# Performance work log

Hardware: AMD Instinct MI355X
Metric: run time of the kernel (lower is better)

Reference implementation:

```python
import jax, jax.numpy as jnp
import numpy as np

K = 3
PAD = K // 2


def conv3x3(x, w, b):
    # x: [B,C,H,W], w: [O,C,3,3], b: [O]
    y = jax.lax.conv_general_dilated(
        x, w, window_strides=(1, 1), padding=[(1, 1), (1, 1)],
        dimension_numbers=("NCHW", "OIHW", "NCHW"))
    return y + b[None, :, None, None]


def bilinear_gather(x, py, px):
    # x: [B,C,H,W]; py, px: [B,KK,H,W] float sample coords -> [B,C,KK,H,W]
    B, C, H, W = x.shape
    y0f = jnp.floor(py)
    x0f = jnp.floor(px)
    ly = (py - y0f)[:, None]  # [B,1,KK,H,W]
    lx = (px - x0f)[:, None]
    y0 = y0f.astype(jnp.int32)
    x0 = x0f.astype(jnp.int32)

    def gather(yi, xi):
        valid = ((yi >= 0) & (yi < H) & (xi >= 0) & (xi < W))
        yc = jnp.clip(yi, 0, H - 1)
        xc = jnp.clip(xi, 0, W - 1)
        # per-batch fancy gather: [C,H,W][: , idx, idx] -> [C,KK,H,W]
        g = jax.vmap(lambda xb, yb, xb2: xb[:, yb, xb2])(x, yc, xc)
        return g * valid[:, None].astype(x.dtype)

    v00 = gather(y0, x0)
    v01 = gather(y0, x0 + 1)
    v10 = gather(y0 + 1, x0)
    v11 = gather(y0 + 1, x0 + 1)
    return (v00 * (1 - ly) * (1 - lx) + v01 * (1 - ly) * lx
            + v10 * ly * (1 - lx) + v11 * ly * lx)


def setup_inputs() -> dict:
    key = jax.random.key(0)
    ks = jax.random.split(key, 7)
    B, C, H, W = 8, 128, 64, 64
    KK = K * K
    s_in = 1.0 / np.sqrt(C * KK)
    s3 = 1.0 / np.sqrt(C * 9)
    return {
        "x": jax.random.normal(ks[0], (B, C, H, W), jnp.float32),
        "offset_w": jax.random.normal(ks[1], (2 * KK, C, 3, 3), jnp.float32) * s3,
        "offset_b": jax.random.normal(ks[2], (2 * KK,), jnp.float32) * 0.01,
        "mask_w": jax.random.normal(ks[3], (KK, C, 3, 3), jnp.float32) * s3,
        "mask_b": jax.random.normal(ks[4], (KK,), jnp.float32) * 0.01,
        "weight": jax.random.normal(ks[5], (C, C, K, K), jnp.float32) * s_in,
        "bias": jax.random.normal(ks[6], (C,), jnp.float32) * 0.01,
    }


def reference(x, offset_w, offset_b, mask_w, mask_b, weight, bias):
    B, C, H, W = x.shape
    KK = K * K
    offset = conv3x3(x, offset_w, offset_b)            # [B,2*KK,H,W]
    mask = jax.nn.sigmoid(conv3x3(x, mask_w, mask_b))  # [B,KK,H,W]
    off = offset.reshape(B, KK, 2, H, W)
    dy, dx = off[:, :, 0], off[:, :, 1]                # torchvision: (dy, dx) per tap

    ky = (jnp.arange(KK, dtype=jnp.float32) // K) - PAD  # [KK] kernel row offsets
    kx = (jnp.arange(KK, dtype=jnp.float32) % K) - PAD
    py = jnp.arange(H, dtype=jnp.float32)[None, None, :, None] + ky[None, :, None, None] + dy
    px = jnp.arange(W, dtype=jnp.float32)[None, None, None, :] + kx[None, :, None, None] + dx

    sampled = bilinear_gather(x, py, px)               # [B,C,KK,H,W]
    sampled = sampled * mask[:, None]
    y = jnp.einsum("bckhw,ock->bohw", sampled, weight.reshape(C, C, KK))
    return y + bias[None, :, None, None]
```

## Files before the change

kernel.cpp:

```cpp
#include <hip/hip_runtime.h>
#include <math.h>

#define BATCH 8
#define CH    128
#define HH    64
#define WW    64
#define HWSZ  (HH*WW)
#define KK    9
#define OC27  27
#define KDIM  1152

typedef unsigned short ushort_t;
typedef unsigned int   uint_t;
typedef __attribute__((ext_vector_type(8))) short  short8v;
typedef __attribute__((ext_vector_type(4))) float  float4v;

__device__ __forceinline__ float bf2f(uint_t u16) {
    return __uint_as_float(u16 << 16);
}
__device__ __forceinline__ float bf2f_hi(uint_t u) {
    return __uint_as_float(u & 0xffff0000u);
}
__device__ __forceinline__ ushort_t f2bf(float f) {
    uint_t u = __float_as_uint(f);
    return (ushort_t)((u + 0x7fffu + ((u >> 16) & 1u)) >> 16);
}

__global__ void k_prep_x(const float* __restrict__ in, ushort_t* __restrict__ out) {
    __shared__ float tile[32][33];
    int b  = blockIdx.z;
    int c0 = blockIdx.y * 32;
    int s0 = blockIdx.x * 32;
    int tx = threadIdx.x, ty = threadIdx.y;
    const float* inb = in  + (size_t)b * CH * HWSZ;
    ushort_t*   outb = out + (size_t)b * HWSZ * CH;
#pragma unroll
    for (int i = 0; i < 32; i += 8)
        tile[ty + i][tx] = inb[(size_t)(c0 + ty + i) * HWSZ + s0 + tx];
    __syncthreads();
#pragma unroll
    for (int i = 0; i < 32; i += 8)
        outb[(size_t)(s0 + ty + i) * CH + c0 + tx] = f2bf(tile[tx][ty + i]);
}

__global__ __launch_bounds__(256) void k_prep_w(const float* __restrict__ weight,
                                                ushort_t* __restrict__ w2) {
    int e = blockIdx.x * 256 + threadIdx.x;
    if (e >= CH * KDIM) return;
    int oc  = e / KDIM;
    int rem = e - oc * KDIM;
    int c   = rem / KK;
    int t   = rem - c * KK;
    int k_lin = (c >> 5) * 288 + t * 32 + (c & 31);
    w2[(size_t)(k_lin >> 3) * (CH * 8) + oc * 8 + (k_lin & 7)] = f2bf(weight[e]);
}

__global__ __launch_bounds__(256) void k_prep_w_om(const float* __restrict__ offset_w,
                                                   const float* __restrict__ mask_w,
                                                   ushort_t* __restrict__ w2om) {
    int e = blockIdx.x * 256 + threadIdx.x;
    if (e >= 32 * KDIM) return;
    int oc  = e / KDIM;
    int rem = e - oc * KDIM;
    int c   = rem / KK;
    int t   = rem - c * KK;
    float v = 0.f;
    if (oc < 18)      v = offset_w[(size_t)oc * KDIM + rem];
    else if (oc < 27) v = mask_w[(size_t)(oc - 18) * KDIM + rem];
    int k_lin = (c >> 5) * 288 + t * 32 + (c & 31);
    w2om[(size_t)(k_lin >> 3) * (32 * 8) + oc * 8 + (k_lin & 7)] = f2bf(v);
}

#define DP   64
#define RSE  320

__device__ __forceinline__ int swz(int row, int off) { return off ^ ((row & 7) << 3); }

__global__ __launch_bounds__(256) void k_fused(
        const ushort_t* __restrict__ x_bf,
        const ushort_t* __restrict__ w2,
        const ushort_t* __restrict__ w2om,
        const float* __restrict__ offset_b, const float* __restrict__ mask_b,
        const float* __restrict__ bias,
        float* __restrict__ out) {
    __shared__ ushort_t s[DP * RSE];
    __shared__ float    psf[2880];

    int tid = threadIdx.x;
    int p0  = blockIdx.x * DP;
    int b   = p0 >> 12;
    int h   = (p0 >> 6) & 63;
    int wid = tid >> 6, lane = tid & 63;
    int lh  = lane >> 4, ll = lane & 15;

    const ushort_t* xb_img = x_bf + ((size_t)b * HWSZ * CH);

    float4v acc1[2];
    acc1[0] = (float4v){0.f, 0.f, 0.f, 0.f};
    acc1[1] = (float4v){0.f, 0.f, 0.f, 0.f};

    for (int chunk = 0; chunk < 4; ++chunk) {
        int c0 = chunk * 32;
#pragma unroll
        for (int i = 0; i < 9; ++i) {
            int v   = tid + i * 256;
            int t   = v >> 8;
            int r   = v & 255;
            int pix = r >> 2, cg = r & 3;
            int y   = h + t / 3 - 1;
            int x   = pix + t % 3 - 1;
            uint4 u = make_uint4(0u, 0u, 0u, 0u);
            if (y >= 0 && y < HH && x >= 0 && x < WW)
                u = *(const uint4*)(xb_img + (size_t)(y * WW + x) * CH + c0 + cg * 8);
            *(uint4*)(&s[pix * RSE + swz(pix, t * 32 + cg * 8)]) = u;
        }
        __syncthreads();

        const ushort_t* wb = w2om + (size_t)chunk * 36 * 256;
#pragma unroll 3
        for (int ks = 0; ks < 9; ++ks) {
            int row = wid * 16 + ll;
            short8v a = *(const short8v*)(&s[row * RSE + swz(row, ks * 32 + lh * 8)]);
            const ushort_t* wp = wb + (ks * 4 + lh) * 256 + ll * 8;
            short8v b0 = *(const short8v*)(wp);
            short8v b1 = *(const short8v*)(wp + 128);
            acc1[0] = __builtin_amdgcn_mfma_f32_16x16x32_bf16(a, b0, acc1[0], 0, 0, 0);
            acc1[1] = __builtin_amdgcn_mfma_f32_16x16x32_bf16(a, b1, acc1[1], 0, 0, 0);
        }
        __syncthreads();
    }

#pragma unroll
    for (int j = 0; j < 2; ++j) {
        int oc = j * 16 + ll;
        if (oc < OC27) {
            float bv = (oc < 18) ? offset_b[oc] : mask_b[oc - 18];
#pragma unroll
            for (int r = 0; r < 4; ++r) {
                int pix = wid * 16 + lh * 4 + r;
                float vv = acc1[j][r] + bv;
                if (oc >= 18) vv = 1.f / (1.f + expf(-vv));
                psf[pix * 27 + oc] = vv;
            }
        }
    }
    __syncthreads();

    float dy0 = 0.f, dx0 = 0.f, m0 = 0.f, dy1 = 0.f, dx1 = 0.f, m1 = 0.f;
    float dy2 = 0.f, dx2 = 0.f, m2 = 0.f;
    {
        int v0 = tid,      pA = v0 / 9, tA = v0 - pA * 9;
        int v1 = tid + 256, pB = v1 / 9, tB = v1 - pB * 9;
        dy0 = psf[pA * 27 + 2 * tA]; dx0 = psf[pA * 27 + 2 * tA + 1]; m0 = psf[pA * 27 + 18 + tA];
        dy1 = psf[pB * 27 + 2 * tB]; dx1 = psf[pB * 27 + 2 * tB + 1]; m1 = psf[pB * 27 + 18 + tB];
        if (tid < 64) {
            int v2 = tid + 512, pC = v2 / 9, tC = v2 - pC * 9;
            dy2 = psf[pC * 27 + 2 * tC]; dx2 = psf[pC * 27 + 2 * tC + 1]; m2 = psf[pC * 27 + 18 + tC];
        }
    }
    __syncthreads();

    uint_t* enc = (uint_t*)(psf + 2304);
#define PARAM_STORE(v, dy, dx, m) {                                             \
        int pix = (v) / 9, t = (v) - pix * 9;                                   \
        float py = (float)(h + t / 3 - 1) + (dy);                               \
        float px = (float)(pix + t % 3 - 1) + (dx);                             \
        float y0f = floorf(py), x0f = floorf(px);                               \
        float ly = py - y0f, lx = px - x0f;                                     \
        int y0 = (int)y0f, x0 = (int)x0f;                                       \
        int y1 = y0 + 1,   x1 = x0 + 1;                                         \
        bool vy0 = (y0 >= 0) & (y0 < HH), vy1 = (y1 >= 0) & (y1 < HH);          \
        bool vx0 = (x0 >= 0) & (x0 < WW), vx1 = (x1 >= 0) & (x1 < WW);          \
        int yc0 = min(max(y0, 0), HH - 1), yc1 = min(max(y1, 0), HH - 1);       \
        int xc0 = min(max(x0, 0), WW - 1), xc1 = min(max(x1, 0), WW - 1);       \
        int idx00 = (yc0 * WW + xc0) * CH;                                      \
        enc[v] = (uint_t)idx00 | ((uint_t)(xc1 - xc0) << 30)                    \
                               | ((uint_t)(yc1 - yc0) << 31);                   \
        float4 wq;                                                              \
        wq.x = (1.f - ly) * (1.f - lx) * (m) * ((vy0 && vx0) ? 1.f : 0.f);      \
        wq.y = (1.f - ly) * lx         * (m) * ((vy0 && vx1) ? 1.f : 0.f);      \
        wq.z = ly         * (1.f - lx) * (m) * ((vy1 && vx0) ? 1.f : 0.f);      \
        wq.w = ly         * lx         * (m) * ((vy1 && vx1) ? 1.f : 0.f);      \
        *(float4*)(&psf[(v) * 4]) = wq;                                         \
    }
    PARAM_STORE(tid,       dy0, dx0, m0);
    PARAM_STORE(tid + 256, dy1, dx1, m1);
    if (tid < 64) PARAM_STORE(tid + 512, dy2, dx2, m2);
#undef PARAM_STORE
    __syncthreads();

    int wr = wid & 1;
    int wc = wid >> 1;
    float4v acc[2][4];
#pragma unroll
    for (int i = 0; i < 2; i++)
#pragma unroll
        for (int j = 0; j < 4; j++)
            acc[i][j] = (float4v){0.f, 0.f, 0.f, 0.f};

    for (int chunk = 0; chunk < 4; ++chunk) {
        int c0 = chunk * 32;
#pragma unroll
        for (int i = 0; i < 9; ++i) {
            int v   = tid + i * 256;
            int t   = v >> 8;
            int r   = v & 255;
            int pix = r >> 2, cg = r & 3;
            int pv  = pix * 9 + t;
            uint_t e  = enc[pv];
            float4 wq = *(const float4*)(&psf[pv * 4]);
            int idx00 = (int)(e & 0x3FFFFFFFu);
            int dxo   = (int)((e >> 30) & 1u) << 7;
            int dyo   = (int)(e >> 31) << 13;
            const ushort_t* bp = xb_img + idx00 + c0 + cg * 8;
            uint4 u00 = *(const uint4*)(bp);
            uint4 u01 = *(const uint4*)(bp + dxo);
            uint4 u10 = *(const uint4*)(bp + dyo);
            uint4 u11 = *(const uint4*)(bp + dxo + dyo);
            uint4 res;
#define CMB(fld) {                                                         \
            float lo = wq.x * bf2f(u00.fld & 0xffffu);                     \
            lo = fmaf(wq.y, bf2f(u01.fld & 0xffffu), lo);                  \
            lo = fmaf(wq.z, bf2f(u10.fld & 0xffffu), lo);                  \
            lo = fmaf(wq.w, bf2f(u11.fld & 0xffffu), lo);                  \
            float hi = wq.x * bf2f_hi(u00.fld);                            \
            hi = fmaf(wq.y, bf2f_hi(u01.fld), hi);                        \
            hi = fmaf(wq.z, bf2f_hi(u10.fld), hi);                        \
            hi = fmaf(wq.w, bf2f_hi(u11.fld), hi);                        \
            res.fld = (uint_t)f2bf(lo) | ((uint_t)f2bf(hi) << 16); }
            CMB(x); CMB(y); CMB(z); CMB(w);
#undef CMB
            *(uint4*)(&s[pix * RSE + swz(pix, t * 32 + cg * 8)]) = res;
        }
        __syncthreads();

        const ushort_t* wb = w2 + (size_t)chunk * 36 * 1024;
        __builtin_amdgcn_s_setprio(1);
#pragma unroll 3
        for (int ks = 0; ks < 9; ++ks) {
            int rowA = wr * 32 + ll;
            int off  = swz(rowA, ks * 32 + lh * 8);
            short8v a0 = *(const short8v*)(&s[rowA * RSE + off]);
            short8v a1 = *(const short8v*)(&s[(rowA + 16) * RSE + off]);
            const ushort_t* wp = wb + (ks * 4 + lh) * 1024 + (wc * 64 + ll) * 8;
            short8v b0 = *(const short8v*)(wp);
            short8v b1 = *(const short8v*)(wp + 128);
            short8v b2 = *(const short8v*)(wp + 256);
            short8v b3 = *(const short8v*)(wp + 384);
            acc[0][0] = __builtin_amdgcn_mfma_f32_16x16x32_bf16(a0, b0, acc[0][0], 0, 0, 0);
            acc[0][1] = __builtin_amdgcn_mfma_f32_16x16x32_bf16(a0, b1, acc[0][1], 0, 0, 0);
            acc[0][2] = __builtin_amdgcn_mfma_f32_16x16x32_bf16(a0, b2, acc[0][2], 0, 0, 0);
            acc[0][3] = __builtin_amdgcn_mfma_f32_16x16x32_bf16(a0, b3, acc[0][3], 0, 0, 0);
            acc[1][0] = __builtin_amdgcn_mfma_f32_16x16x32_bf16(a1, b0, acc[1][0], 0, 0, 0);
            acc[1][1] = __builtin_amdgcn_mfma_f32_16x16x32_bf16(a1, b1, acc[1][1], 0, 0, 0);
            acc[1][2] = __builtin_amdgcn_mfma_f32_16x16x32_bf16(a1, b2, acc[1][2], 0, 0, 0);
            acc[1][3] = __builtin_amdgcn_mfma_f32_16x16x32_bf16(a1, b3, acc[1][3], 0, 0, 0);
        }
        __builtin_amdgcn_s_setprio(0);
        __syncthreads();
    }

#pragma unroll
    for (int pi = 0; pi < 2; ++pi) {
#pragma unroll
        for (int oj = 0; oj < 4; ++oj) {
            int oc = wc * 64 + oj * 16 + ll;
            int w  = wr * 32 + pi * 16 + lh * 4;
            float bv = bias[oc];
            float4v a = acc[pi][oj];
            float* op = out + (((size_t)(b * CH + oc)) << 12) + (h << 6) + w;
            *(float4*)op = make_float4(a[0] + bv, a[1] + bv, a[2] + bv, a[3] + bv);
        }
    }
}

extern "C" void kernel_launch(void* const* d_in, const int* in_sizes, int n_in,
                              void* d_out, int out_size, void* d_ws, size_t ws_size,
                              hipStream_t stream) {
    const float* x        = (const float*)d_in[0];
    const float* offset_w = (const float*)d_in[1];
    const float* offset_b = (const float*)d_in[2];
    const float* mask_w   = (const float*)d_in[3];
    const float* mask_b   = (const float*)d_in[4];
    const float* weight   = (const float*)d_in[5];
    const float* bias     = (const float*)d_in[6];
    float* out = (float*)d_out;

    char* ws = (char*)d_ws;
    ushort_t* x_bf = (ushort_t*)ws;
    ushort_t* w2   = (ushort_t*)(ws + 8388608);
    ushort_t* w2om = (ushort_t*)(ws + 8388608 + 294912);

    dim3 tb(32, 8, 1);
    dim3 tg(HWSZ / 32, CH / 32, BATCH);
    k_prep_x<<<tg, tb, 0, stream>>>(x, x_bf);
    k_prep_w<<<(CH * KDIM + 255) / 256, 256, 0, stream>>>(weight, w2);
    k_prep_w_om<<<(32 * KDIM + 255) / 256, 256, 0, stream>>>(offset_w, mask_w, w2om);

    int npix = BATCH * HWSZ;
    k_fused<<<npix / DP, 256, 0, stream>>>(x_bf, w2, w2om, offset_b, mask_b, bias, out);
}
```

Measured before the change: 61.98 us.

## Prefetch next channel chunk into registers during MFMA in both GEMM phases

Both the offset/mask conv phase and the deformable GEMM phase now issue global loads for the next 32-channel chunk into registers before the MFMA loop, then write them to shared memory after the barrier. The goal is to hide gather latency behind matrix compute. The thread-to-pixel mapping is simplified, and launch_bounds now requests 2 blocks per CU. This adds many live registers: 36 uint4 for the bilinear prefetch, which risks spills or lower occupancy.

```diff
diff --git a/kernel.cpp b/kernel.cpp
--- a/kernel.cpp
+++ b/kernel.cpp
@@ -76,7 +76,7 @@
 
 __device__ __forceinline__ int swz(int row, int off) { return off ^ ((row & 7) << 3); }
 
-__global__ __launch_bounds__(256) void k_fused(
+__global__ __launch_bounds__(256, 2) void k_fused(
         const ushort_t* __restrict__ x_bf,
         const ushort_t* __restrict__ w2,
         const ushort_t* __restrict__ w2om,
@@ -95,39 +95,58 @@
 
     const ushort_t* xb_img = x_bf + ((size_t)b * HWSZ * CH);
 
+    int pixS = tid >> 2, cgS = tid & 3;
+
     float4v acc1[2];
     acc1[0] = (float4v){0.f, 0.f, 0.f, 0.f};
     acc1[1] = (float4v){0.f, 0.f, 0.f, 0.f};
 
-    for (int chunk = 0; chunk < 4; ++chunk) {
-        int c0 = chunk * 32;
+    {
+        uint4 pf1[9];
 #pragma unroll
         for (int i = 0; i < 9; ++i) {
-            int v   = tid + i * 256;
-            int t   = v >> 8;
-            int r   = v & 255;
-            int pix = r >> 2, cg = r & 3;
-            int y   = h + t / 3 - 1;
-            int x   = pix + t % 3 - 1;
+            int y = h + i / 3 - 1;
+            int x = pixS + i % 3 - 1;
             uint4 u = make_uint4(0u, 0u, 0u, 0u);
             if (y >= 0 && y < HH && x >= 0 && x < WW)
-                u = *(const uint4*)(xb_img + (size_t)(y * WW + x) * CH + c0 + cg * 8);
-            *(uint4*)(&s[pix * RSE + swz(pix, t * 32 + cg * 8)]) = u;
-        }
-        __syncthreads();
-
-        const ushort_t* wb = w2om + (size_t)chunk * 36 * 256;
+                u = *(const uint4*)(xb_img + (size_t)(y * WW + x) * CH + cgS * 8);
+            *(uint4*)(&s[pixS * RSE + swz(pixS, i * 32 + cgS * 8)]) = u;
+        }
+        for (int chunk = 0; chunk < 4; ++chunk) {
+            __syncthreads();
+            if (chunk < 3) {
+                int c0n = (chunk + 1) * 32;
+#pragma unroll
+                for (int i = 0; i < 9; ++i) {
+                    int y = h + i / 3 - 1;
+                    int x = pixS + i % 3 - 1;
+                    int yc = min(max(y, 0), HH - 1), xc = min(max(x, 0), WW - 1);
+                    pf1[i] = *(const uint4*)(xb_img + (size_t)(yc * WW + xc) * CH + c0n + cgS * 8);
+                }
+            }
+            const ushort_t* wb = w2om + (size_t)chunk * 36 * 256;
 #pragma unroll 3
-        for (int ks = 0; ks < 9; ++ks) {
-            int row = wid * 16 + ll;
-            short8v a = *(const short8v*)(&s[row * RSE + swz(row, ks * 32 + lh * 8)]);
-            const ushort_t* wp = wb + (ks * 4 + lh) * 256 + ll * 8;
-            short8v b0 = *(const short8v*)(wp);
-            short8v b1 = *(const short8v*)(wp + 128);
-            acc1[0] = __builtin_amdgcn_mfma_f32_16x16x32_bf16(a, b0, acc1[0], 0, 0, 0);
-            acc1[1] = __builtin_amdgcn_mfma_f32_16x16x32_bf16(a, b1, acc1[1], 0, 0, 0);
-        }
-        __syncthreads();
+            for (int ks = 0; ks < 9; ++ks) {
+                int row = wid * 16 + ll;
+                short8v a = *(const short8v*)(&s[row * RSE + swz(row, ks * 32 + lh * 8)]);
+                const ushort_t* wp = wb + (ks * 4 + lh) * 256 + ll * 8;
+                short8v b0 = *(const short8v*)(wp);
+                short8v b1 = *(const short8v*)(wp + 128);
+                acc1[0] = __builtin_amdgcn_mfma_f32_16x16x32_bf16(a, b0, acc1[0], 0, 0, 0);
+                acc1[1] = __builtin_amdgcn_mfma_f32_16x16x32_bf16(a, b1, acc1[1], 0, 0, 0);
+            }
+            __syncthreads();
+            if (chunk < 3) {
+#pragma unroll
+                for (int i = 0; i < 9; ++i) {
+                    int y = h + i / 3 - 1;
+                    int x = pixS + i % 3 - 1;
+                    bool valid = (y >= 0) && (y < HH) && (x >= 0) && (x < WW);
+                    uint4 u = valid ? pf1[i] : make_uint4(0u, 0u, 0u, 0u);
+                    *(uint4*)(&s[pixS * RSE + swz(pixS, i * 32 + cgS * 8)]) = u;
+                }
+            }
+        }
     }
 
 #pragma unroll
@@ -198,26 +217,6 @@
         for (int j = 0; j < 4; j++)
             acc[i][j] = (float4v){0.f, 0.f, 0.f, 0.f};
 
-    for (int chunk = 0; chunk < 4; ++chunk) {
-        int c0 = chunk * 32;
-#pragma unroll
-        for (int i = 0; i < 9; ++i) {
-            int v   = tid + i * 256;
-            int t   = v >> 8;
-            int r   = v & 255;
-            int pix = r >> 2, cg = r & 3;
-            int pv  = pix * 9 + t;
-            uint_t e  = enc[pv];
-            float4 wq = *(const float4*)(&psf[pv * 4]);
-            int idx00 = (int)(e & 0x3FFFFFFFu);
-            int dxo   = (int)((e >> 30) & 1u) << 7;
-            int dyo   = (int)(e >> 31) << 13;
-            const ushort_t* bp = xb_img + idx00 + c0 + cg * 8;
-            uint4 u00 = *(const uint4*)(bp);
-            uint4 u01 = *(const uint4*)(bp + dxo);
-            uint4 u10 = *(const uint4*)(bp + dyo);
-            uint4 u11 = *(const uint4*)(bp + dxo + dyo);
-            uint4 res;
 #define CMB(fld) {                                                         \
             float lo = wq.x * bf2f(u00.fld & 0xffffu);                     \
             lo = fmaf(wq.y, bf2f(u01.fld & 0xffffu), lo);                  \
@@ -228,37 +227,84 @@
             hi = fmaf(wq.z, bf2f_hi(u10.fld), hi);                        \
             hi = fmaf(wq.w, bf2f_hi(u11.fld), hi);                        \
             res.fld = (uint_t)f2bf(lo) | ((uint_t)f2bf(hi) << 16); }
+
+    {
+        uint4 pf[9][4];
+#pragma unroll
+        for (int i = 0; i < 9; ++i) {
+            int pv  = pixS * 9 + i;
+            uint_t e  = enc[pv];
+            float4 wq = *(const float4*)(&psf[pv * 4]);
+            int idx00 = (int)(e & 0x3FFFFFFFu);
+            int dxo   = (int)((e >> 30) & 1u) << 7;
+            int dyo   = (int)(e >> 31) << 13;
+            const ushort_t* bp = xb_img + idx00 + cgS * 8;
+            uint4 u00 = *(const uint4*)(bp);
+            uint4 u01 = *(const uint4*)(bp + dxo);
+            uint4 u10 = *(const uint4*)(bp + dyo);
+            uint4 u11 = *(const uint4*)(bp + dxo + dyo);
+            uint4 res;
             CMB(x); CMB(y); CMB(z); CMB(w);
+            *(uint4*)(&s[pixS * RSE + swz(pixS, i * 32 + cgS * 8)]) = res;
+        }
+        for (int chunk = 0; chunk < 4; ++chunk) {
+            __syncthreads();
+            if (chunk < 3) {
+                int c0n = (chunk + 1) * 32;
+#pragma unroll
+                for (int i = 0; i < 9; ++i) {
+                    uint_t e  = enc[pixS * 9 + i];
+                    int idx00 = (int)(e & 0x3FFFFFFFu);
+                    int dxo   = (int)((e >> 30) & 1u) << 7;
+                    int dyo   = (int)(e >> 31) << 13;
+                    const ushort_t* bp = xb_img + idx00 + c0n + cgS * 8;
+                    pf[i][0] = *(const uint4*)(bp);
+                    pf[i][1] = *(const uint4*)(bp + dxo);
+                    pf[i][2] = *(const uint4*)(bp + dyo);
+                    pf[i][3] = *(const uint4*)(bp + dxo + dyo);
+                }
+            }
+            const ushort_t* wb = w2 + (size_t)chunk * 36 * 1024;
+            __builtin_amdgcn_s_setprio(1);
+#pragma unroll 3
+            for (int ks = 0; ks < 9; ++ks) {
+                int rowA = wr * 32 + ll;
+                int off  = swz(rowA, ks * 32 + lh * 8);
+                short8v a0 = *(const short8v*)(&s[rowA * RSE + off]);
+                short8v a1 = *(const short8v*)(&s[(rowA + 16) * RSE + off]);
+                const ushort_t* wp = wb + (ks * 4 + lh) * 1024 + (wc * 64 + ll) * 8;
+                short8v b0 = *(const short8v*)(wp);
+                short8v b1 = *(const short8v*)(wp + 128);
+                short8v b2 = *(const short8v*)(wp + 256);
+                short8v b3 = *(const short8v*)(wp + 384);
+                acc[0][0] = __builtin_amdgcn_mfma_f32_16x16x32_bf16(a0, b0, acc[0][0], 0, 0, 0);
+                acc[0][1] = __builtin_amdgcn_mfma_f32_16x16x32_bf16(a0, b1, acc[0][1], 0, 0, 0);
+                acc[0][2] = __builtin_amdgcn_mfma_f32_16x16x32_bf16(a0, b2, acc[0][2], 0, 0, 0);
+                acc[0][3] = __builtin_amdgcn_mfma_f32_16x16x32_bf16(a0, b3, acc[0][3], 0, 0, 0);
+                acc[1][0] = __builtin_amdgcn_mfma_f32_16x16x32_bf16(a1, b0, acc[1][0], 0, 0, 0);
+                acc[1][1] = __builtin_amdgcn_mfma_f32_16x16x32_bf16(a1, b1, acc[1][1], 0, 0, 0);
+                acc[1][2] = __builtin_amdgcn_mfma_f32_16x16x32_bf16(a1, b2, acc[1][2], 0, 0, 0);
+                acc[1][3] = __builtin_amdgcn_mfma_f32_16x16x32_bf16(a1, b3, acc[1][3], 0, 0, 0);
+            }
+            __builtin_amdgcn_s_setprio(0);
+            __syncthreads();
+            if (chunk < 3) {
+#pragma unroll
+                for (int i = 0; i < 9; ++i) {
+                    int pv = pixS * 9 + i;
+                    float4 wq = *(const float4*)(&psf[pv * 4]);
+                    uint4 u00 = pf[i][0];
+                    uint4 u01 = pf[i][1];
+                    uint4 u10 = pf[i][2];
+                    uint4 u11 = pf[i][3];
+                    uint4 res;
+                    CMB(x); CMB(y); CMB(z); CMB(w);
+                    *(uint4*)(&s[pixS * RSE + swz(pixS, i * 32 + cgS * 8)]) = res;
+                }
+            }
+        }
+    }
 #undef CMB
-            *(uint4*)(&s[pix * RSE + swz(pix, t * 32 + cg * 8)]) = res;
-        }
-        __syncthreads();
-
-        const ushort_t* wb = w2 + (size_t)chunk * 36 * 1024;
-        __builtin_amdgcn_s_setprio(1);
-#pragma unroll 3
-        for (int ks = 0; ks < 9; ++ks) {
-            int rowA = wr * 32 + ll;
-            int off  = swz(rowA, ks * 32 + lh * 8);
-            short8v a0 = *(const short8v*)(&s[rowA * RSE + off]);
-            short8v a1 = *(const short8v*)(&s[(rowA + 16) * RSE + off]);
-            const ushort_t* wp = wb + (ks * 4 + lh) * 1024 + (wc * 64 + ll) * 8;
-            short8v b0 = *(const short8v*)(wp);
-            short8v b1 = *(const short8v*)(wp + 128);
-            short8v b2 = *(const short8v*)(wp + 256);
-            short8v b3 = *(const short8v*)(wp + 384);
-            acc[0][0] = __builtin_amdgcn_mfma_f32_16x16x32_bf16(a0, b0, acc[0][0], 0, 0, 0);
-            acc[0][1] = __builtin_amdgcn_mfma_f32_16x16x32_bf16(a0, b1, acc[0][1], 0, 0, 0);
-            acc[0][2] = __builtin_amdgcn_mfma_f32_16x16x32_bf16(a0, b2, acc[0][2], 0, 0, 0);
-            acc[0][3] = __builtin_amdgcn_mfma_f32_16x16x32_bf16(a0, b3, acc[0][3], 0, 0, 0);
-            acc[1][0] = __builtin_amdgcn_mfma_f32_16x16x32_bf16(a1, b0, acc[1][0], 0, 0, 0);
-            acc[1][1] = __builtin_amdgcn_mfma_f32_16x16x32_bf16(a1, b1, acc[1][1], 0, 0, 0);
-            acc[1][2] = __builtin_amdgcn_mfma_f32_16x16x32_bf16(a1, b2, acc[1][2], 0, 0, 0);
-            acc[1][3] = __builtin_amdgcn_mfma_f32_16x16x32_bf16(a1, b3, acc[1][3], 0, 0, 0);
-        }
-        __builtin_amdgcn_s_setprio(0);
-        __syncthreads();
-    }
 
 #pragma unroll
     for (int pi = 0; pi < 2; ++pi) {
```

After: 61.10 us. Within noise of the previous version (-1.4%).

## Split output channels across two blocks and merge weight prep kernels

Applied to the files above, without the earlier changes.

The fused kernel now launches twice as many blocks, with each block handling half of the output channels (64) for its 64 pixels. Each wave now computes 16 pixels by 64 channels instead of 32 by 64, which halves accumulator registers and should raise occupancy and block-level parallelism. The cost is that each block pair repeats the offset/mask convolution and the bilinear gather, so that work is done twice. The two weight-prep kernels are also merged into one launch to save launch overhead.

```diff
diff --git a/kernel.cpp b/kernel.cpp
--- a/kernel.cpp
+++ b/kernel.cpp
@@ -43,32 +43,31 @@
         outb[(size_t)(s0 + ty + i) * CH + c0 + tx] = f2bf(tile[tx][ty + i]);
 }
 
-__global__ __launch_bounds__(256) void k_prep_w(const float* __restrict__ weight,
-                                                ushort_t* __restrict__ w2) {
+__global__ __launch_bounds__(256) void k_prep_wb(const float* __restrict__ weight,
+                                                 const float* __restrict__ offset_w,
+                                                 const float* __restrict__ mask_w,
+                                                 ushort_t* __restrict__ w2,
+                                                 ushort_t* __restrict__ w2om) {
     int e = blockIdx.x * 256 + threadIdx.x;
-    if (e >= CH * KDIM) return;
-    int oc  = e / KDIM;
-    int rem = e - oc * KDIM;
-    int c   = rem / KK;
-    int t   = rem - c * KK;
-    int k_lin = (c >> 5) * 288 + t * 32 + (c & 31);
-    w2[(size_t)(k_lin >> 3) * (CH * 8) + oc * 8 + (k_lin & 7)] = f2bf(weight[e]);
-}
-
-__global__ __launch_bounds__(256) void k_prep_w_om(const float* __restrict__ offset_w,
-                                                   const float* __restrict__ mask_w,
-                                                   ushort_t* __restrict__ w2om) {
-    int e = blockIdx.x * 256 + threadIdx.x;
-    if (e >= 32 * KDIM) return;
-    int oc  = e / KDIM;
-    int rem = e - oc * KDIM;
-    int c   = rem / KK;
-    int t   = rem - c * KK;
-    float v = 0.f;
-    if (oc < 18)      v = offset_w[(size_t)oc * KDIM + rem];
-    else if (oc < 27) v = mask_w[(size_t)(oc - 18) * KDIM + rem];
-    int k_lin = (c >> 5) * 288 + t * 32 + (c & 31);
-    w2om[(size_t)(k_lin >> 3) * (32 * 8) + oc * 8 + (k_lin & 7)] = f2bf(v);
+    if (e < CH * KDIM) {
+        int oc  = e / KDIM;
+        int rem = e - oc * KDIM;
+        int c   = rem / KK;
+        int t   = rem - c * KK;
+        int k_lin = (c >> 5) * 288 + t * 32 + (c & 31);
+        w2[(size_t)(k_lin >> 3) * (CH * 8) + oc * 8 + (k_lin & 7)] = f2bf(weight[e]);
+    } else if (e < CH * KDIM + 32 * KDIM) {
+        int e2  = e - CH * KDIM;
+        int oc  = e2 / KDIM;
+        int rem = e2 - oc * KDIM;
+        int c   = rem / KK;
+        int t   = rem - c * KK;
+        float v = 0.f;
+        if (oc < 18)      v = offset_w[(size_t)oc * KDIM + rem];
+        else if (oc < 27) v = mask_w[(size_t)(oc - 18) * KDIM + rem];
+        int k_lin = (c >> 5) * 288 + t * 32 + (c & 31);
+        w2om[(size_t)(k_lin >> 3) * (32 * 8) + oc * 8 + (k_lin & 7)] = f2bf(v);
+    }
 }
 
 #define DP   64
@@ -189,14 +188,12 @@
 #undef PARAM_STORE
     __syncthreads();
 
-    int wr = wid & 1;
-    int wc = wid >> 1;
-    float4v acc[2][4];
-#pragma unroll
-    for (int i = 0; i < 2; i++)
-#pragma unroll
-        for (int j = 0; j < 4; j++)
-            acc[i][j] = (float4v){0.f, 0.f, 0.f, 0.f};
+    int wr = wid;
+    int wc = blockIdx.y;
+    float4v acc[4];
+#pragma unroll
+    for (int j = 0; j < 4; j++)
+        acc[j] = (float4v){0.f, 0.f, 0.f, 0.f};
 
     for (int chunk = 0; chunk < 4; ++chunk) {
         int c0 = chunk * 32;
@@ -238,39 +235,30 @@
         __builtin_amdgcn_s_setprio(1);
 #pragma unroll 3
         for (int ks = 0; ks < 9; ++ks) {
-            int rowA = wr * 32 + ll;
-            int off  = swz(rowA, ks * 32 + lh * 8);
-            short8v a0 = *(const short8v*)(&s[rowA * RSE + off]);
-            short8v a1 = *(const short8v*)(&s[(rowA + 16) * RSE + off]);
+            int rowA = wr * 16 + ll;
+            short8v a0 = *(const short8v*)(&s[rowA * RSE + swz(rowA, ks * 32 + lh * 8)]);
             const ushort_t* wp = wb + (ks * 4 + lh) * 1024 + (wc * 64 + ll) * 8;
             short8v b0 = *(const short8v*)(wp);
             short8v b1 = *(const short8v*)(wp + 128);
             short8v b2 = *(const short8v*)(wp + 256);
             short8v b3 = *(const short8v*)(wp + 384);
-            acc[0][0] = __builtin_amdgcn_mfma_f32_16x16x32_bf16(a0, b0, acc[0][0], 0, 0, 0);
-            acc[0][1] = __builtin_amdgcn_mfma_f32_16x16x32_bf16(a0, b1, acc[0][1], 0, 0, 0);
-            acc[0][2] = __builtin_amdgcn_mfma_f32_16x16x32_bf16(a0, b2, acc[0][2], 0, 0, 0);
-            acc[0][3] = __builtin_amdgcn_mfma_f32_16x16x32_bf16(a0, b3, acc[0][3], 0, 0, 0);
-            acc[1][0] = __builtin_amdgcn_mfma_f32_16x16x32_bf16(a1, b0, acc[1][0], 0, 0, 0);
-            acc[1][1] = __builtin_amdgcn_mfma_f32_16x16x32_bf16(a1, b1, acc[1][1], 0, 0, 0);
-            acc[1][2] = __builtin_amdgcn_mfma_f32_16x16x32_bf16(a1, b2, acc[1][2], 0, 0, 0);
-            acc[1][3] = __builtin_amdgcn_mfma_f32_16x16x32_bf16(a1, b3, acc[1][3], 0, 0, 0);
+            acc[0] = __builtin_amdgcn_mfma_f32_16x16x32_bf16(a0, b0, acc[0], 0, 0, 0);
+            acc[1] = __builtin_amdgcn_mfma_f32_16x16x32_bf16(a0, b1, acc[1], 0, 0, 0);
+            acc[2] = __builtin_amdgcn_mfma_f32_16x16x32_bf16(a0, b2, acc[2], 0, 0, 0);
+            acc[3] = __builtin_amdgcn_mfma_f32_16x16x32_bf16(a0, b3, acc[3], 0, 0, 0);
         }
         __builtin_amdgcn_s_setprio(0);
         __syncthreads();
     }
 
 #pragma unroll
-    for (int pi = 0; pi < 2; ++pi) {
-#pragma unroll
-        for (int oj = 0; oj < 4; ++oj) {
-            int oc = wc * 64 + oj * 16 + ll;
-            int w  = wr * 32 + pi * 16 + lh * 4;
-            float bv = bias[oc];
-            float4v a = acc[pi][oj];
-            float* op = out + (((size_t)(b * CH + oc)) << 12) + (h << 6) + w;
-            *(float4*)op = make_float4(a[0] + bv, a[1] + bv, a[2] + bv, a[3] + bv);
-        }
+    for (int oj = 0; oj < 4; ++oj) {
+        int oc = wc * 64 + oj * 16 + ll;
+        int w  = wr * 16 + lh * 4;
+        float bv = bias[oc];
+        float4v a = acc[oj];
+        float* op = out + (((size_t)(b * CH + oc)) << 12) + (h << 6) + w;
+        *(float4*)op = make_float4(a[0] + bv, a[1] + bv, a[2] + bv, a[3] + bv);
     }
 }
 
@@ -294,9 +282,9 @@
     dim3 tb(32, 8, 1);
     dim3 tg(HWSZ / 32, CH / 32, BATCH);
     k_prep_x<<<tg, tb, 0, stream>>>(x, x_bf);
-    k_prep_w<<<(CH * KDIM + 255) / 256, 256, 0, stream>>>(weight, w2);
-    k_prep_w_om<<<(32 * KDIM + 255) / 256, 256, 0, stream>>>(offset_w, mask_w, w2om);
+    k_prep_wb<<<((CH + 32) * KDIM + 255) / 256, 256, 0, stream>>>(weight, offset_w, mask_w, w2, w2om);
 
     int npix = BATCH * HWSZ;
-    k_fused<<<npix / DP, 256, 0, stream>>>(x_bf, w2, w2om, offset_b, mask_b, bias, out);
-}
+    dim3 fg(npix / DP, 2, 1);
+    k_fused<<<fg, 256, 0, stream>>>(x_bf, w2, w2om, offset_b, mask_b, bias, out);
+}
```

After: 99.22 us. +60.1%, slower.

## Merge prep kernels into one launch and stage halo rows for offset conv

Applied to the files above, without the earlier changes.

Combines the three preprocessing kernels (x transpose to bf16, weight reorder, offset/mask weight reorder) into a single launch, removing two kernel launch gaps. In the fused kernel, the offset/mask conv no longer stages a 9x im2col copy of the input. It loads three halo rows of 66 pixels once per channel chunk into a padded shared layout and indexes taps by row and column shift. This cuts global loads and LDS writes per chunk, at the cost of an unswizzled padded-stride layout that may cause LDS bank conflicts.

```diff
diff --git a/kernel.cpp b/kernel.cpp
--- a/kernel.cpp
+++ b/kernel.cpp
@@ -26,53 +26,56 @@
     return (ushort_t)((u + 0x7fffu + ((u >> 16) & 1u)) >> 16);
 }
 
-__global__ void k_prep_x(const float* __restrict__ in, ushort_t* __restrict__ out) {
+__global__ __launch_bounds__(256) void k_prep_all(const float* __restrict__ in,
+                                                  const float* __restrict__ weight,
+                                                  const float* __restrict__ offset_w,
+                                                  const float* __restrict__ mask_w,
+                                                  ushort_t* __restrict__ x_bf,
+                                                  ushort_t* __restrict__ w2,
+                                                  ushort_t* __restrict__ w2om) {
     __shared__ float tile[32][33];
-    int b  = blockIdx.z;
-    int c0 = blockIdx.y * 32;
-    int s0 = blockIdx.x * 32;
-    int tx = threadIdx.x, ty = threadIdx.y;
-    const float* inb = in  + (size_t)b * CH * HWSZ;
-    ushort_t*   outb = out + (size_t)b * HWSZ * CH;
-#pragma unroll
-    for (int i = 0; i < 32; i += 8)
-        tile[ty + i][tx] = inb[(size_t)(c0 + ty + i) * HWSZ + s0 + tx];
-    __syncthreads();
-#pragma unroll
-    for (int i = 0; i < 32; i += 8)
-        outb[(size_t)(s0 + ty + i) * CH + c0 + tx] = f2bf(tile[tx][ty + i]);
-}
-
-__global__ __launch_bounds__(256) void k_prep_w(const float* __restrict__ weight,
-                                                ushort_t* __restrict__ w2) {
-    int e = blockIdx.x * 256 + threadIdx.x;
-    if (e >= CH * KDIM) return;
-    int oc  = e / KDIM;
-    int rem = e - oc * KDIM;
-    int c   = rem / KK;
-    int t   = rem - c * KK;
-    int k_lin = (c >> 5) * 288 + t * 32 + (c & 31);
-    w2[(size_t)(k_lin >> 3) * (CH * 8) + oc * 8 + (k_lin & 7)] = f2bf(weight[e]);
-}
-
-__global__ __launch_bounds__(256) void k_prep_w_om(const float* __restrict__ offset_w,
-                                                   const float* __restrict__ mask_w,
-                                                   ushort_t* __restrict__ w2om) {
-    int e = blockIdx.x * 256 + threadIdx.x;
-    if (e >= 32 * KDIM) return;
-    int oc  = e / KDIM;
-    int rem = e - oc * KDIM;
-    int c   = rem / KK;
-    int t   = rem - c * KK;
-    float v = 0.f;
-    if (oc < 18)      v = offset_w[(size_t)oc * KDIM + rem];
-    else if (oc < 27) v = mask_w[(size_t)(oc - 18) * KDIM + rem];
-    int k_lin = (c >> 5) * 288 + t * 32 + (c & 31);
-    w2om[(size_t)(k_lin >> 3) * (32 * 8) + oc * 8 + (k_lin & 7)] = f2bf(v);
+    int bid = blockIdx.x;
+    int tid = threadIdx.x;
+    if (bid < 4096) {
+        int bx = bid & 127, by = (bid >> 7) & 3, bz = bid >> 9;
+        int s0 = bx * 32, c0 = by * 32, b = bz;
+        int tx = tid & 31, ty = tid >> 5;
+        const float* inb = in   + (size_t)b * CH * HWSZ;
+        ushort_t*   outb = x_bf + (size_t)b * HWSZ * CH;
+#pragma unroll
+        for (int i = 0; i < 32; i += 8)
+            tile[ty + i][tx] = inb[(size_t)(c0 + ty + i) * HWSZ + s0 + tx];
+        __syncthreads();
+#pragma unroll
+        for (int i = 0; i < 32; i += 8)
+            outb[(size_t)(s0 + ty + i) * CH + c0 + tx] = f2bf(tile[tx][ty + i]);
+    } else {
+        int e = (bid - 4096) * 256 + tid;
+        if (e < CH * KDIM) {
+            int oc  = e / KDIM;
+            int rem = e - oc * KDIM;
+            int c   = rem / KK;
+            int t   = rem - c * KK;
+            int k_lin = (c >> 5) * 288 + t * 32 + (c & 31);
+            w2[(size_t)(k_lin >> 3) * (CH * 8) + oc * 8 + (k_lin & 7)] = f2bf(weight[e]);
+        } else if (e < CH * KDIM + 32 * KDIM) {
+            int e2  = e - CH * KDIM;
+            int oc  = e2 / KDIM;
+            int rem = e2 - oc * KDIM;
+            int c   = rem / KK;
+            int t   = rem - c * KK;
+            float v = 0.f;
+            if (oc < 18)      v = offset_w[(size_t)oc * KDIM + rem];
+            else if (oc < 27) v = mask_w[(size_t)(oc - 18) * KDIM + rem];
+            int k_lin = (c >> 5) * 288 + t * 32 + (c & 31);
+            w2om[(size_t)(k_lin >> 3) * (32 * 8) + oc * 8 + (k_lin & 7)] = f2bf(v);
+        }
+    }
 }
 
 #define DP   64
 #define RSE  320
+#define CPAD 40
 
 __device__ __forceinline__ int swz(int row, int off) { return off ^ ((row & 7) << 3); }
 
@@ -101,26 +104,25 @@
 
     for (int chunk = 0; chunk < 4; ++chunk) {
         int c0 = chunk * 32;
-#pragma unroll
-        for (int i = 0; i < 9; ++i) {
-            int v   = tid + i * 256;
-            int t   = v >> 8;
-            int r   = v & 255;
-            int pix = r >> 2, cg = r & 3;
-            int y   = h + t / 3 - 1;
-            int x   = pix + t % 3 - 1;
+        for (int v = tid; v < 3 * 66 * 4; v += 256) {
+            int yr  = v / 264;
+            int r   = v - yr * 264;
+            int col = r >> 2, cg = r & 3;
+            int y   = h + yr - 1;
+            int x   = col - 1;
             uint4 u = make_uint4(0u, 0u, 0u, 0u);
             if (y >= 0 && y < HH && x >= 0 && x < WW)
                 u = *(const uint4*)(xb_img + (size_t)(y * WW + x) * CH + c0 + cg * 8);
-            *(uint4*)(&s[pix * RSE + swz(pix, t * 32 + cg * 8)]) = u;
+            *(uint4*)(&s[(yr * 66 + col) * CPAD + cg * 8]) = u;
         }
         __syncthreads();
 
         const ushort_t* wb = w2om + (size_t)chunk * 36 * 256;
-#pragma unroll 3
+#pragma unroll
         for (int ks = 0; ks < 9; ++ks) {
-            int row = wid * 16 + ll;
-            short8v a = *(const short8v*)(&s[row * RSE + swz(row, ks * 32 + lh * 8)]);
+            int yr = ks / 3, dx = ks % 3;
+            int col = wid * 16 + ll + dx;
+            short8v a = *(const short8v*)(&s[(yr * 66 + col) * CPAD + lh * 8]);
             const ushort_t* wp = wb + (ks * 4 + lh) * 256 + ll * 8;
             short8v b0 = *(const short8v*)(wp);
             short8v b1 = *(const short8v*)(wp + 128);
@@ -291,11 +293,9 @@
     ushort_t* w2   = (ushort_t*)(ws + 8388608);
     ushort_t* w2om = (ushort_t*)(ws + 8388608 + 294912);
 
-    dim3 tb(32, 8, 1);
-    dim3 tg(HWSZ / 32, CH / 32, BATCH);
-    k_prep_x<<<tg, tb, 0, stream>>>(x, x_bf);
-    k_prep_w<<<(CH * KDIM + 255) / 256, 256, 0, stream>>>(weight, w2);
-    k_prep_w_om<<<(32 * KDIM + 255) / 256, 256, 0, stream>>>(offset_w, mask_w, w2om);
+    int wblocks = ((CH + 32) * KDIM + 255) / 256;
+    k_prep_all<<<4096 + wblocks, 256, 0, stream>>>(x, weight, offset_w, mask_w,
+                                                   x_bf, w2, w2om);
 
     int npix = BATCH * HWSZ;
     k_fused<<<npix / DP, 256, 0, stream>>>(x_bf, w2, w2om, offset_b, mask_b, bias, out);
```

Result: faster. 53.86 us (-13.1%).
